# Performance work log

Hardware: AMD Instinct MI355X
Metric: run time of the kernel (lower is better)

The kernel has to match this reference:

```python
import jax, jax.numpy as jnp
import numpy as np

D_MODEL = 1024
NUM_HEADS = 16
HEAD_DIM = D_MODEL // NUM_HEADS
B, S = 2, 2048


def setup_inputs() -> dict:
    key = jax.random.key(0)
    ks = jax.random.split(key, 9)
    scale = 1.0 / np.sqrt(D_MODEL)
    return {
        "x": jax.random.normal(ks[0], (B, S, D_MODEL), jnp.float32),
        "y": jax.random.normal(ks[1], (B, S, D_MODEL), jnp.float32),
        "mask": jnp.zeros((B, S, S), jnp.float32),
        "Wkv": jax.random.normal(ks[2], (D_MODEL, 2 * D_MODEL), jnp.float32) * scale,
        "bkv": jnp.zeros((2 * D_MODEL,), jnp.float32),
        "Wq": jax.random.normal(ks[3], (D_MODEL, D_MODEL), jnp.float32) * scale,
        "bq": jnp.zeros((D_MODEL,), jnp.float32),
        "Wo": jax.random.normal(ks[4], (D_MODEL, D_MODEL), jnp.float32) * scale,
        "bo": jnp.zeros((D_MODEL,), jnp.float32),
    }


def reference(x, y, mask, Wkv, bkv, Wq, bq, Wo, bo):
    b, s, d = x.shape
    h, hd = NUM_HEADS, HEAD_DIM
    # projections
    kv = x @ Wkv + bkv                       # [B, S, 2D]
    q = y @ Wq + bq                          # [B, S, D]
    kv = kv.reshape(b, s, h, 2 * hd).transpose(0, 2, 1, 3)  # [B, H, S, 2hd]
    q = q.reshape(b, s, h, hd).transpose(0, 2, 1, 3)        # [B, H, S, hd]
    k, v = kv[..., :hd], kv[..., hd:]
    # scaled dot-product attention with additive per-batch mask
    scaled = jnp.einsum("bhqd,bhkd->bhqk", q, k) / jnp.sqrt(jnp.float32(hd))
    scaled = scaled + mask[:, None, :, :]    # mask [B,S,S] broadcast over heads
    attn = jax.nn.softmax(scaled, axis=-1)
    vals = jnp.einsum("bhqk,bhkd->bhqd", attn, v)            # [B, H, S, hd]
    vals = vals.transpose(0, 2, 1, 3).reshape(b, s, d)       # [B, S, D]
    return vals @ Wo + bo
```

## Files before the change

kernel.cpp:

```cpp
#include <hip/hip_runtime.h>
#include <hip/hip_bf16.h>

#define D_MODEL 1024
#define NHEADS 16
#define HD 64
#define BATCH 2
#define SEQ 2048
#define BS (BATCH*SEQ)

typedef __bf16 bf16;
typedef bf16 bf16x4 __attribute__((ext_vector_type(4)));
typedef bf16 bf16x8 __attribute__((ext_vector_type(8)));
typedef float f32x4 __attribute__((ext_vector_type(4)));

#define AS1 __attribute__((address_space(1)))
#define AS3 __attribute__((address_space(3)))

__device__ __forceinline__ void gload_lds16(const void* g, void* l) {
  __builtin_amdgcn_global_load_lds((AS1 const unsigned int*)g, (AS3 unsigned int*)l, 16, 0, 0);
}

__device__ __forceinline__ float exp2_fast(float x) {
  float r;
  asm("v_exp_f32 %0, %1\n\ts_nop 1" : "=v"(r) : "v"(x));
  return r;
}

__global__ void cvt_bf16(const float* __restrict__ in, bf16* __restrict__ out, int n8) {
  int i = blockIdx.x * blockDim.x + threadIdx.x;
  int stride = gridDim.x * blockDim.x;
  for (; i < n8; i += stride) {
    const float4* p = (const float4*)(in + (size_t)i * 8);
    float4 a = p[0], b = p[1];
    bf16x8 o;
    o[0]=(bf16)a.x; o[1]=(bf16)a.y; o[2]=(bf16)a.z; o[3]=(bf16)a.w;
    o[4]=(bf16)b.x; o[5]=(bf16)b.y; o[6]=(bf16)b.z; o[7]=(bf16)b.w;
    *(bf16x8*)(out + (size_t)i * 8) = o;
  }
}

__global__ void transpose_cvt(const float* __restrict__ in, bf16* __restrict__ out, int R, int C) {
  __shared__ bf16 tile[64][72];
  const int t = threadIdx.x;
  const int r0 = blockIdx.x * 64;
  const int c0 = blockIdx.y * 64;
  {
    int r = t >> 2, cc = (t & 3) * 16;
    const float* src = in + (size_t)(r0 + r) * C + c0 + cc;
    #pragma unroll
    for (int j = 0; j < 16; j += 4) {
      float4 v = *(const float4*)(src + j);
      tile[r][cc + j + 0] = (bf16)v.x;
      tile[r][cc + j + 1] = (bf16)v.y;
      tile[r][cc + j + 2] = (bf16)v.z;
      tile[r][cc + j + 3] = (bf16)v.w;
    }
  }
  __syncthreads();
  {
    int c = t >> 2, rr = (t & 3) * 16;
    bf16* dst = out + (size_t)(c0 + c) * R + r0 + rr;
    bf16x8 o0, o1;
    #pragma unroll
    for (int j = 0; j < 8; j++) { o0[j] = tile[rr + j][c]; o1[j] = tile[rr + 8 + j][c]; }
    *(bf16x8*)dst = o0;
    *(bf16x8*)(dst + 8) = o1;
  }
}

__global__ void mask_scan(const float* __restrict__ mask, int n4, int* __restrict__ flag) {
  int i = blockIdx.x * blockDim.x + threadIdx.x;
  int stride = gridDim.x * blockDim.x;
  int any = 0;
  for (; i < n4; i += stride) {
    float4 v = *(const float4*)(mask + (size_t)i * 4);
    if (v.x != 0.f || v.y != 0.f || v.z != 0.f || v.w != 0.f) any = 1;
  }
  if (__ballot(any) && (threadIdx.x & 63) == 0) atomicOr(flag, 1);
}

template <typename OutT, int MODE>
__global__ __launch_bounds__(256)
void gemm_bt(const bf16* __restrict__ A, const bf16* __restrict__ Bt,
             const float* __restrict__ bias, OutT* __restrict__ C,
             bf16* __restrict__ Vt, int M, int N, int K, float scale) {
  __shared__ char lds[32768];
  char* Alds = lds;
  char* Blds = lds + 16384;
  const int t = threadIdx.x;
  const int lane = t & 63;
  const int wid = t >> 6;
  const int m0 = blockIdx.x * 128;
  const int n0 = blockIdx.y * 128;
  const int wr = wid >> 1, wc = wid & 1;

  f32x4 acc[4][4] = {};

  int rowL[4], colL[4];
  #pragma unroll
  for (int i = 0; i < 4; i++) {
    int L = t * 16 + i * 4096;
    int r = L >> 7;
    rowL[i] = r;
    colL[i] = (L & 127) ^ ((r & 7) << 4);
  }
  const char* Ab = (const char*)A;
  const char* Bb = (const char*)Bt;
  const size_t rs = (size_t)K * 2;

  for (int k0 = 0; k0 < K; k0 += 64) {
    #pragma unroll
    for (int i = 0; i < 4; i++) {
      gload_lds16(Ab + (size_t)(m0 + rowL[i]) * rs + (size_t)k0 * 2 + colL[i],
                  Alds + i * 4096 + t * 16);
      gload_lds16(Bb + (size_t)(n0 + rowL[i]) * rs + (size_t)k0 * 2 + colL[i],
                  Blds + i * 4096 + t * 16);
    }
    __syncthreads();
    #pragma unroll
    for (int kb = 0; kb < 2; kb++) {
      bf16x8 af[4], bfr[4];
      #pragma unroll
      for (int m = 0; m < 4; m++) {
        int r = wr * 64 + m * 16 + (lane & 15);
        int cb = (kb * 64 + ((lane >> 4) << 4)) ^ ((r & 7) << 4);
        af[m] = *(const bf16x8*)(Alds + r * 128 + cb);
      }
      #pragma unroll
      for (int n = 0; n < 4; n++) {
        int r = wc * 64 + n * 16 + (lane & 15);
        int cb = (kb * 64 + ((lane >> 4) << 4)) ^ ((r & 7) << 4);
        bfr[n] = *(const bf16x8*)(Blds + r * 128 + cb);
      }
      #pragma unroll
      for (int m = 0; m < 4; m++)
        #pragma unroll
        for (int n = 0; n < 4; n++)
          acc[m][n] = __builtin_amdgcn_mfma_f32_16x16x32_bf16(af[m], bfr[n], acc[m][n], 0, 0, 0);
    }
    __syncthreads();
  }

  if (MODE == 1 && wc == 1) {
    const int h = n0 >> 7;
    const int bb = m0 >> 11;
    #pragma unroll
    for (int n = 0; n < 4; n++) {
      const int d = n * 16 + (lane & 15);
      const int cg = n0 + 64 + d;
      const float bv = bias[cg];
      bf16* vrow = Vt + ((size_t)((bb * NHEADS + h) * HD + d)) * SEQ;
      #pragma unroll
      for (int m = 0; m < 4; m++) {
        const int rb = m0 + wr * 64 + m * 16 + ((lane >> 4) << 2);
        const int s = rb & (SEQ - 1);
        bf16x4 v;
        #pragma unroll
        for (int j = 0; j < 4; j++) v[j] = (bf16)((acc[m][n][j] + bv) * scale);
        *(bf16x4*)(vrow + s) = v;
      }
    }
  } else {
    #pragma unroll
    for (int m = 0; m < 4; m++) {
      const int rb = m0 + wr * 64 + m * 16 + ((lane >> 4) << 2);
      #pragma unroll
      for (int n = 0; n < 4; n++) {
        const int cg = n0 + wc * 64 + n * 16 + (lane & 15);
        const float bv = bias[cg];
        #pragma unroll
        for (int j = 0; j < 4; j++) {
          C[(size_t)(rb + j) * N + cg] = (OutT)((acc[m][n][j] + bv) * scale);
        }
      }
    }
  }
}

__global__ __launch_bounds__(256)
void attn_kernel(const bf16* __restrict__ Qb, const bf16* __restrict__ KV,
                 const bf16* __restrict__ Vt, const float* __restrict__ mask,
                 const int* __restrict__ flag, bf16* __restrict__ vals) {
  __shared__ char lds[49152];
  const int t = threadIdx.x;
  const int lane = t & 63;
  const int wid = t >> 6;
  const int g = lane >> 4;
  const int lq = lane & 15;
  char* Pw = lds + 32768 + wid * 4096;

  int wg = ((blockIdx.x & 7) << 6) | (blockIdx.x >> 3);
  const int qt = wg & 15;
  const int h = (wg >> 4) & 15;
  const int b = wg >> 8;
  const int q0 = qt * 128 + wid * 32;
  const bool use_mask = (*flag) != 0;

  bf16x8 qf[2][2];
  #pragma unroll
  for (int m = 0; m < 2; m++)
    #pragma unroll
    for (int kb = 0; kb < 2; kb++) {
      int r = q0 + m * 16 + lq;
      qf[m][kb] = *(const bf16x8*)(Qb + (size_t)(b * SEQ + r) * D_MODEL + h * HD + kb * 32 + g * 8);
    }

  f32x4 oacc[2][4] = {};
  float mrun[2], lrun[2];
  mrun[0] = mrun[1] = -1e30f;
  lrun[0] = lrun[1] = 0.f;

  int kvOff[2][4];
  #pragma unroll
  for (int kb = 0; kb < 2; kb++)
    #pragma unroll
    for (int n = 0; n < 4; n++) {
      int r = n * 16 + lq;
      kvOff[kb][n] = r * 128 + ((kb * 64 + (g << 4)) ^ ((r & 7) << 4));
    }
  int pROff[2][2];
  #pragma unroll
  for (int m = 0; m < 2; m++)
    #pragma unroll
    for (int kb = 0; kb < 2; kb++) {
      int r = m * 16 + lq;
      pROff[m][kb] = r * 128 + ((kb * 64 + (g << 4)) ^ ((r & 7) << 4));
    }
  int pWOff[2][4];
  #pragma unroll
  for (int m = 0; m < 2; m++) {
    int r = m * 16 + lq;
    int swz = (r & 7) << 4;
    #pragma unroll
    for (int n = 0; n < 4; n++)
      pWOff[m][n] = r * 128 + ((n * 32 + g * 8) ^ swz);
  }

  int rowL[2], colL[2];
  #pragma unroll
  for (int i = 0; i < 2; i++) {
    int L = t * 16 + i * 4096;
    int r = L >> 7;
    rowL[i] = r;
    colL[i] = (L & 127) ^ ((r & 7) << 4);
  }
  const char* KVb = (const char*)KV;
  const char* Vtb = (const char*)Vt;

  auto stage = [&](int kt, int c) {
    const int kv0 = kt * 64;
    char* Kb = lds + c * 16384;
    char* Vb = Kb + 8192;
    #pragma unroll
    for (int i = 0; i < 2; i++) {
      gload_lds16(KVb + (size_t)(b * SEQ + kv0 + rowL[i]) * (2 * D_MODEL * 2) + h * 256 + colL[i],
                  Kb + i * 4096 + t * 16);
      gload_lds16(Vtb + (size_t)((b * NHEADS + h) * HD + rowL[i]) * (SEQ * 2) + kv0 * 2 + colL[i],
                  Vb + i * 4096 + t * 16);
    }
  };

  stage(0, 0);
  __syncthreads();
  int cur = 0;

  const int NT = SEQ / 64;
  for (int kt = 0; kt < NT; kt++) {
    if (kt + 1 < NT) stage(kt + 1, cur ^ 1);
    char* Klds = lds + cur * 16384;
    char* Vlds = Klds + 8192;
    const int kv0 = kt * 64;

    f32x4 sacc[2][4] = {};
    __builtin_amdgcn_s_setprio(1);
    #pragma unroll
    for (int kb = 0; kb < 2; kb++) {
      bf16x8 kf[4];
      #pragma unroll
      for (int n = 0; n < 4; n++)
        kf[n] = *(const bf16x8*)(Klds + kvOff[kb][n]);
      #pragma unroll
      for (int m = 0; m < 2; m++)
        #pragma unroll
        for (int n = 0; n < 4; n++)
          sacc[m][n] = __builtin_amdgcn_mfma_f32_16x16x32_bf16(kf[n], qf[m][kb], sacc[m][n], 0, 0, 0);
    }
    __builtin_amdgcn_s_setprio(0);

    if (use_mask) {
      #pragma unroll
      for (int m = 0; m < 2; m++) {
        int qg = q0 + m * 16 + lq;
        const float* mrow = mask + ((size_t)b * SEQ + qg) * SEQ + kv0;
        #pragma unroll
        for (int n = 0; n < 4; n++)
          #pragma unroll
          for (int j = 0; j < 4; j++)
            sacc[m][n][j] += mrow[n * 16 + g * 4 + j] * 1.44269504f;
      }
    }

    float pm[2];
    #pragma unroll
    for (int m = 0; m < 2; m++) {
      float a0 = fmaxf(fmaxf(sacc[m][0][0], sacc[m][0][1]), fmaxf(sacc[m][0][2], sacc[m][0][3]));
      float a1 = fmaxf(fmaxf(sacc[m][1][0], sacc[m][1][1]), fmaxf(sacc[m][1][2], sacc[m][1][3]));
      float a2 = fmaxf(fmaxf(sacc[m][2][0], sacc[m][2][1]), fmaxf(sacc[m][2][2], sacc[m][2][3]));
      float a3 = fmaxf(fmaxf(sacc[m][3][0], sacc[m][3][1]), fmaxf(sacc[m][3][2], sacc[m][3][3]));
      float v = fmaxf(fmaxf(a0, a1), fmaxf(a2, a3));
      v = fmaxf(v, __shfl_xor(v, 16, 64));
      v = fmaxf(v, __shfl_xor(v, 32, 64));
      pm[m] = v;
    }

    int nogrow = (pm[0] <= mrun[0] + 8.f) && (pm[1] <= mrun[1] + 8.f);
    if (!__all(nogrow)) {
      #pragma unroll
      for (int m = 0; m < 2; m++) {
        float mn = fmaxf(mrun[m], pm[m]);
        float sf = exp2_fast(mrun[m] - mn);
        mrun[m] = mn;
        lrun[m] *= sf;
        float sfj[4];
        #pragma unroll
        for (int j = 0; j < 4; j++) sfj[j] = __shfl(sf, (g << 2) + j, 64);
        #pragma unroll
        for (int n = 0; n < 4; n++)
          #pragma unroll
          for (int j = 0; j < 4; j++)
            oacc[m][n][j] *= sfj[j];
      }
    }

    #pragma unroll
    for (int m = 0; m < 2; m++) {
      float rsn[4];
      #pragma unroll
      for (int n = 0; n < 4; n++) {
        float e0 = exp2_fast(sacc[m][n][0] - mrun[m]);
        float e1 = exp2_fast(sacc[m][n][1] - mrun[m]);
        float e2 = exp2_fast(sacc[m][n][2] - mrun[m]);
        float e3 = exp2_fast(sacc[m][n][3] - mrun[m]);
        rsn[n] = (e0 + e1) + (e2 + e3);
        bf16x4 p = {(bf16)e0, (bf16)e1, (bf16)e2, (bf16)e3};
        *(bf16x4*)(Pw + pWOff[m][n]) = p;
      }
      lrun[m] += (rsn[0] + rsn[1]) + (rsn[2] + rsn[3]);
    }

    asm volatile("s_waitcnt lgkmcnt(0)" ::: "memory");
    __builtin_amdgcn_sched_barrier(0);

    __builtin_amdgcn_s_setprio(1);
    #pragma unroll
    for (int kb = 0; kb < 2; kb++) {
      bf16x8 pf[2], vf[4];
      #pragma unroll
      for (int m = 0; m < 2; m++)
        pf[m] = *(const bf16x8*)(Pw + pROff[m][kb]);
      #pragma unroll
      for (int n = 0; n < 4; n++)
        vf[n] = *(const bf16x8*)(Vlds + kvOff[kb][n]);
      #pragma unroll
      for (int m = 0; m < 2; m++)
        #pragma unroll
        for (int n = 0; n < 4; n++)
          oacc[m][n] = __builtin_amdgcn_mfma_f32_16x16x32_bf16(pf[m], vf[n], oacc[m][n], 0, 0, 0);
    }
    __builtin_amdgcn_s_setprio(0);

    __syncthreads();
    cur ^= 1;
  }

  #pragma unroll
  for (int m = 0; m < 2; m++) {
    lrun[m] += __shfl_xor(lrun[m], 16, 64);
    lrun[m] += __shfl_xor(lrun[m], 32, 64);
  }

  #pragma unroll
  for (int m = 0; m < 2; m++) {
    float inv[4];
    #pragma unroll
    for (int j = 0; j < 4; j++)
      inv[j] = 1.f / __shfl(lrun[m], (g << 2) + j, 64);
    #pragma unroll
    for (int n = 0; n < 4; n++) {
      int cg = h * HD + n * 16 + lq;
      #pragma unroll
      for (int j = 0; j < 4; j++) {
        int rg = b * SEQ + q0 + m * 16 + g * 4 + j;
        vals[(size_t)rg * D_MODEL + cg] = (bf16)(oacc[m][n][j] * inv[j]);
      }
    }
  }
}

extern "C" void kernel_launch(void* const* d_in, const int* in_sizes, int n_in,
                              void* d_out, int out_size, void* d_ws, size_t ws_size,
                              hipStream_t stream) {
  const float* x    = (const float*)d_in[0];
  const float* y    = (const float*)d_in[1];
  const float* mask = (const float*)d_in[2];
  const float* Wkv  = (const float*)d_in[3];
  const float* bkv  = (const float*)d_in[4];
  const float* Wq   = (const float*)d_in[5];
  const float* bq   = (const float*)d_in[6];
  const float* Wo   = (const float*)d_in[7];
  const float* bo   = (const float*)d_in[8];
  float* out = (float*)d_out;

  char* ws = (char*)d_ws;
  bf16* xb   = (bf16*)(ws);
  bf16* yb   = (bf16*)(ws + (8ull << 20));
  bf16* Wkvt = (bf16*)(ws + (16ull << 20));
  bf16* Wqt  = (bf16*)(ws + (20ull << 20));
  bf16* Wot  = (bf16*)(ws + (22ull << 20));
  bf16* KVb  = (bf16*)(ws + (24ull << 20));
  bf16* Qbuf = (bf16*)(ws + (40ull << 20));
  bf16* Vt   = (bf16*)(ws + (48ull << 20));
  bf16* vals = (bf16*)(ws + (56ull << 20));
  int*  flag = (int*)(ws + (64ull << 20));

  const float QSCL = 0.125f * 1.44269504f;

  hipMemsetAsync(flag, 0, 4, stream);
  mask_scan<<<2048, 256, 0, stream>>>(mask, BATCH * SEQ * SEQ / 4, flag);
  cvt_bf16<<<2048, 256, 0, stream>>>(x, xb, BS * D_MODEL / 8);
  cvt_bf16<<<2048, 256, 0, stream>>>(y, yb, BS * D_MODEL / 8);
  transpose_cvt<<<dim3(16, 32), 256, 0, stream>>>(Wkv, Wkvt, 1024, 2048);
  transpose_cvt<<<dim3(16, 16), 256, 0, stream>>>(Wq, Wqt, 1024, 1024);
  transpose_cvt<<<dim3(16, 16), 256, 0, stream>>>(Wo, Wot, 1024, 1024);
  gemm_bt<bf16, 1><<<dim3(32, 16), 256, 0, stream>>>(xb, Wkvt, bkv, KVb, Vt, 4096, 2048, 1024, 1.0f);
  gemm_bt<bf16, 0><<<dim3(32, 8), 256, 0, stream>>>(yb, Wqt, bq, Qbuf, nullptr, 4096, 1024, 1024, QSCL);
  attn_kernel<<<512, 256, 0, stream>>>(Qbuf, KVb, Vt, mask, flag, vals);
  gemm_bt<float, 0><<<dim3(32, 8), 256, 0, stream>>>(vals, Wot, bo, out, nullptr, 4096, 1024, 1024, 1.0f);
}
```

Baseline: 160.3 us.

## Load K/V fragments directly from global memory in single-wave attention blocks

Restructures the attention kernel from 4-wave workgroups that stage K/V tiles into double-buffered shared memory into single-wave workgroups (4x as many blocks) that read K and V MFMA fragments straight from global memory into registers. This removes the LDS staging, the block-wide barriers and the LDS read traffic, and lets each wave run independently. In exchange, K/V reuse across the four waves of a block is lost, so global/L2 traffic rises about fourfold and the loads are no longer prefetched one tile ahead, which exposes memory latency unless occupancy hides it.

```diff
diff --git a/kernel.cpp b/kernel.cpp
--- a/kernel.cpp
+++ b/kernel.cpp
@@ -177,23 +177,20 @@
   }
 }
 
-__global__ __launch_bounds__(256)
+__global__ __launch_bounds__(64)
 void attn_kernel(const bf16* __restrict__ Qb, const bf16* __restrict__ KV,
                  const bf16* __restrict__ Vt, const float* __restrict__ mask,
                  const int* __restrict__ flag, bf16* __restrict__ vals) {
-  __shared__ char lds[49152];
-  const int t = threadIdx.x;
-  const int lane = t & 63;
-  const int wid = t >> 6;
+  __shared__ char Pw[4096];
+  const int lane = threadIdx.x;
   const int g = lane >> 4;
   const int lq = lane & 15;
-  char* Pw = lds + 32768 + wid * 4096;
-
-  int wg = ((blockIdx.x & 7) << 6) | (blockIdx.x >> 3);
-  const int qt = wg & 15;
-  const int h = (wg >> 4) & 15;
-  const int b = wg >> 8;
-  const int q0 = qt * 128 + wid * 32;
+
+  int wg = ((blockIdx.x & 7) << 8) | (blockIdx.x >> 3);
+  const int qt = wg & 63;
+  const int h = (wg >> 6) & 15;
+  const int b = wg >> 10;
+  const int q0 = qt * 32;
   const bool use_mask = (*flag) != 0;
 
   bf16x8 qf[2][2];
@@ -210,14 +207,6 @@
   mrun[0] = mrun[1] = -1e30f;
   lrun[0] = lrun[1] = 0.f;
 
-  int kvOff[2][4];
-  #pragma unroll
-  for (int kb = 0; kb < 2; kb++)
-    #pragma unroll
-    for (int n = 0; n < 4; n++) {
-      int r = n * 16 + lq;
-      kvOff[kb][n] = r * 128 + ((kb * 64 + (g << 4)) ^ ((r & 7) << 4));
-    }
   int pROff[2][2];
   #pragma unroll
   for (int m = 0; m < 2; m++)
@@ -236,56 +225,37 @@
       pWOff[m][n] = r * 128 + ((n * 32 + g * 8) ^ swz);
   }
 
-  int rowL[2], colL[2];
-  #pragma unroll
-  for (int i = 0; i < 2; i++) {
-    int L = t * 16 + i * 4096;
-    int r = L >> 7;
-    rowL[i] = r;
-    colL[i] = (L & 127) ^ ((r & 7) << 4);
-  }
-  const char* KVb = (const char*)KV;
-  const char* Vtb = (const char*)Vt;
-
-  auto stage = [&](int kt, int c) {
-    const int kv0 = kt * 64;
-    char* Kb = lds + c * 16384;
-    char* Vb = Kb + 8192;
-    #pragma unroll
-    for (int i = 0; i < 2; i++) {
-      gload_lds16(KVb + (size_t)(b * SEQ + kv0 + rowL[i]) * (2 * D_MODEL * 2) + h * 256 + colL[i],
-                  Kb + i * 4096 + t * 16);
-      gload_lds16(Vtb + (size_t)((b * NHEADS + h) * HD + rowL[i]) * (SEQ * 2) + kv0 * 2 + colL[i],
-                  Vb + i * 4096 + t * 16);
-    }
-  };
-
-  stage(0, 0);
-  __syncthreads();
-  int cur = 0;
+  const bf16* Kb = KV + (size_t)(b * SEQ) * (2 * D_MODEL) + h * 128;
+  const bf16* Vb = Vt + (size_t)((b * NHEADS + h) * HD) * SEQ;
 
   const int NT = SEQ / 64;
   for (int kt = 0; kt < NT; kt++) {
-    if (kt + 1 < NT) stage(kt + 1, cur ^ 1);
-    char* Klds = lds + cur * 16384;
-    char* Vlds = Klds + 8192;
     const int kv0 = kt * 64;
+
+    bf16x8 kf[2][4];
+    #pragma unroll
+    for (int kb = 0; kb < 2; kb++)
+      #pragma unroll
+      for (int n = 0; n < 4; n++)
+        kf[kb][n] = *(const bf16x8*)(Kb + (size_t)(kv0 + n * 16 + lq) * (2 * D_MODEL) + kb * 32 + g * 8);
 
     f32x4 sacc[2][4] = {};
     __builtin_amdgcn_s_setprio(1);
     #pragma unroll
-    for (int kb = 0; kb < 2; kb++) {
-      bf16x8 kf[4];
+    for (int kb = 0; kb < 2; kb++)
+      #pragma unroll
+      for (int m = 0; m < 2; m++)
+        #pragma unroll
+        for (int n = 0; n < 4; n++)
+          sacc[m][n] = __builtin_amdgcn_mfma_f32_16x16x32_bf16(kf[kb][n], qf[m][kb], sacc[m][n], 0, 0, 0);
+    __builtin_amdgcn_s_setprio(0);
+
+    bf16x8 vf[2][4];
+    #pragma unroll
+    for (int kb = 0; kb < 2; kb++)
       #pragma unroll
       for (int n = 0; n < 4; n++)
-        kf[n] = *(const bf16x8*)(Klds + kvOff[kb][n]);
-      #pragma unroll
-      for (int m = 0; m < 2; m++)
-        #pragma unroll
-        for (int n = 0; n < 4; n++)
-          sacc[m][n] = __builtin_amdgcn_mfma_f32_16x16x32_bf16(kf[n], qf[m][kb], sacc[m][n], 0, 0, 0);
-    }
-    __builtin_amdgcn_s_setprio(0);
+        vf[kb][n] = *(const bf16x8*)(Vb + (size_t)(n * 16 + lq) * SEQ + kv0 + kb * 32 + g * 8);
 
     if (use_mask) {
       #pragma unroll
@@ -348,29 +318,20 @@
       lrun[m] += (rsn[0] + rsn[1]) + (rsn[2] + rsn[3]);
     }
 
-    asm volatile("s_waitcnt lgkmcnt(0)" ::: "memory");
-    __builtin_amdgcn_sched_barrier(0);
-
     __builtin_amdgcn_s_setprio(1);
     #pragma unroll
     for (int kb = 0; kb < 2; kb++) {
-      bf16x8 pf[2], vf[4];
+      bf16x8 pf[2];
       #pragma unroll
       for (int m = 0; m < 2; m++)
         pf[m] = *(const bf16x8*)(Pw + pROff[m][kb]);
       #pragma unroll
-      for (int n = 0; n < 4; n++)
-        vf[n] = *(const bf16x8*)(Vlds + kvOff[kb][n]);
-      #pragma unroll
       for (int m = 0; m < 2; m++)
         #pragma unroll
         for (int n = 0; n < 4; n++)
-          oacc[m][n] = __builtin_amdgcn_mfma_f32_16x16x32_bf16(pf[m], vf[n], oacc[m][n], 0, 0, 0);
+          oacc[m][n] = __builtin_amdgcn_mfma_f32_16x16x32_bf16(pf[m], vf[kb][n], oacc[m][n], 0, 0, 0);
     }
     __builtin_amdgcn_s_setprio(0);
-
-    __syncthreads();
-    cur ^= 1;
   }
 
   #pragma unroll
@@ -434,6 +395,6 @@
   transpose_cvt<<<dim3(16, 16), 256, 0, stream>>>(Wo, Wot, 1024, 1024);
   gemm_bt<bf16, 1><<<dim3(32, 16), 256, 0, stream>>>(xb, Wkvt, bkv, KVb, Vt, 4096, 2048, 1024, 1.0f);
   gemm_bt<bf16, 0><<<dim3(32, 8), 256, 0, stream>>>(yb, Wqt, bq, Qbuf, nullptr, 4096, 1024, 1024, QSCL);
-  attn_kernel<<<512, 256, 0, stream>>>(Qbuf, KVb, Vt, mask, flag, vals);
+  attn_kernel<<<2048, 64, 0, stream>>>(Qbuf, KVb, Vt, mask, flag, vals);
   gemm_bt<float, 0><<<dim3(32, 8), 256, 0, stream>>>(vals, Wot, bo, out, nullptr, 4096, 1024, 1024, 1.0f);
 }
```

After: 218.0 us. +36.0%, slower.

## Merge preprocessing kernels and fuse K/V and Q projection GEMMs into one launch

Applied to the files above, without the earlier changes.

The mask scan, the x/y bf16 conversions and the three weight transpose-converts now run as one block-indexed prep kernel instead of six launches. The KV and Q projection GEMMs share a single launch, with a 32x24 grid that dispatches on blockIdx.y. The goal is to cut launch overhead and tail idle time between small kernels and to give the GPU a larger, fuller grid for the projections. The cost is branchy block dispatch and some extra register pressure in the combined GEMM epilogue; KV tiles still store the K half row-major, while wc==1 waves write V transposed.

```diff
diff --git a/kernel.cpp b/kernel.cpp
--- a/kernel.cpp
+++ b/kernel.cpp
@@ -26,64 +26,190 @@
   return r;
 }
 
-__global__ void cvt_bf16(const float* __restrict__ in, bf16* __restrict__ out, int n8) {
-  int i = blockIdx.x * blockDim.x + threadIdx.x;
-  int stride = gridDim.x * blockDim.x;
-  for (; i < n8; i += stride) {
+__global__ __launch_bounds__(256)
+void prep_kernel(const float* __restrict__ x, const float* __restrict__ y,
+                 const float* __restrict__ mask,
+                 const float* __restrict__ Wkv, const float* __restrict__ Wq,
+                 const float* __restrict__ Wo,
+                 bf16* __restrict__ xb, bf16* __restrict__ yb,
+                 bf16* __restrict__ Wkvt, bf16* __restrict__ Wqt,
+                 bf16* __restrict__ Wot, int* __restrict__ flag) {
+  __shared__ bf16 tile[64][72];
+  const int blk = blockIdx.x;
+  const int t = threadIdx.x;
+
+  if (blk < 4096) {
+    const float* in = (blk < 2048) ? x : y;
+    bf16* out = (blk < 2048) ? xb : yb;
+    int i = (blk & 2047) * 256 + t;
     const float4* p = (const float4*)(in + (size_t)i * 8);
     float4 a = p[0], b = p[1];
     bf16x8 o;
     o[0]=(bf16)a.x; o[1]=(bf16)a.y; o[2]=(bf16)a.z; o[3]=(bf16)a.w;
     o[4]=(bf16)b.x; o[5]=(bf16)b.y; o[6]=(bf16)b.z; o[7]=(bf16)b.w;
     *(bf16x8*)(out + (size_t)i * 8) = o;
-  }
-}
-
-__global__ void transpose_cvt(const float* __restrict__ in, bf16* __restrict__ out, int R, int C) {
-  __shared__ bf16 tile[64][72];
+  } else if (blk < 5120) {
+    const float* tin; bf16* tout; int C, tt;
+    if (blk < 4608)      { tin = Wkv; tout = Wkvt; C = 2048; tt = blk - 4096; }
+    else if (blk < 4864) { tin = Wq;  tout = Wqt;  C = 1024; tt = blk - 4608; }
+    else                 { tin = Wo;  tout = Wot;  C = 1024; tt = blk - 4864; }
+    const int R = 1024;
+    const int r0 = (tt & 15) * 64;
+    const int c0 = (tt >> 4) * 64;
+    {
+      int r = t >> 2, cc = (t & 3) * 16;
+      const float* src = tin + (size_t)(r0 + r) * C + c0 + cc;
+      #pragma unroll
+      for (int j = 0; j < 16; j += 4) {
+        float4 v = *(const float4*)(src + j);
+        tile[r][cc + j + 0] = (bf16)v.x;
+        tile[r][cc + j + 1] = (bf16)v.y;
+        tile[r][cc + j + 2] = (bf16)v.z;
+        tile[r][cc + j + 3] = (bf16)v.w;
+      }
+    }
+    __syncthreads();
+    {
+      int c = t >> 2, rr = (t & 3) * 16;
+      bf16* dst = tout + (size_t)(c0 + c) * R + r0 + rr;
+      bf16x8 o0, o1;
+      #pragma unroll
+      for (int j = 0; j < 8; j++) { o0[j] = tile[rr + j][c]; o1[j] = tile[rr + 8 + j][c]; }
+      *(bf16x8*)dst = o0;
+      *(bf16x8*)(dst + 8) = o1;
+    }
+  } else {
+    const int n4 = BATCH * SEQ * SEQ / 4;
+    int i = (blk - 5120) * 256 + t;
+    const int stride = 1024 * 256;
+    int any = 0;
+    for (; i < n4; i += stride) {
+      float4 v = *(const float4*)(mask + (size_t)i * 4);
+      if (v.x != 0.f || v.y != 0.f || v.z != 0.f || v.w != 0.f) any = 1;
+    }
+    if (__ballot(any) && (t & 63) == 0) atomicOr(flag, 1);
+  }
+}
+
+__global__ __launch_bounds__(256)
+void qkv_gemm(const bf16* __restrict__ xb, const bf16* __restrict__ yb,
+              const bf16* __restrict__ Wkvt, const bf16* __restrict__ Wqt,
+              const float* __restrict__ bkv, const float* __restrict__ bq,
+              bf16* __restrict__ KVb, bf16* __restrict__ Qbuf,
+              bf16* __restrict__ Vt, float QSCL) {
+  __shared__ char lds[32768];
+  char* Alds = lds;
+  char* Blds = lds + 16384;
+  const int K = 1024;
   const int t = threadIdx.x;
-  const int r0 = blockIdx.x * 64;
-  const int c0 = blockIdx.y * 64;
-  {
-    int r = t >> 2, cc = (t & 3) * 16;
-    const float* src = in + (size_t)(r0 + r) * C + c0 + cc;
-    #pragma unroll
-    for (int j = 0; j < 16; j += 4) {
-      float4 v = *(const float4*)(src + j);
-      tile[r][cc + j + 0] = (bf16)v.x;
-      tile[r][cc + j + 1] = (bf16)v.y;
-      tile[r][cc + j + 2] = (bf16)v.z;
-      tile[r][cc + j + 3] = (bf16)v.w;
-    }
-  }
-  __syncthreads();
-  {
-    int c = t >> 2, rr = (t & 3) * 16;
-    bf16* dst = out + (size_t)(c0 + c) * R + r0 + rr;
-    bf16x8 o0, o1;
-    #pragma unroll
-    for (int j = 0; j < 8; j++) { o0[j] = tile[rr + j][c]; o1[j] = tile[rr + 8 + j][c]; }
-    *(bf16x8*)dst = o0;
-    *(bf16x8*)(dst + 8) = o1;
-  }
-}
-
-__global__ void mask_scan(const float* __restrict__ mask, int n4, int* __restrict__ flag) {
-  int i = blockIdx.x * blockDim.x + threadIdx.x;
-  int stride = gridDim.x * blockDim.x;
-  int any = 0;
-  for (; i < n4; i += stride) {
-    float4 v = *(const float4*)(mask + (size_t)i * 4);
-    if (v.x != 0.f || v.y != 0.f || v.z != 0.f || v.w != 0.f) any = 1;
-  }
-  if (__ballot(any) && (threadIdx.x & 63) == 0) atomicOr(flag, 1);
-}
-
-template <typename OutT, int MODE>
+  const int lane = t & 63;
+  const int wid = t >> 6;
+  const int m0 = blockIdx.x * 128;
+  const int by = blockIdx.y;
+  const bool isQ = by >= 16;
+  const int n0 = (isQ ? by - 16 : by) * 128;
+  const bf16* A = isQ ? yb : xb;
+  const bf16* Bt = isQ ? Wqt : Wkvt;
+  const int wr = wid >> 1, wc = wid & 1;
+
+  f32x4 acc[4][4] = {};
+
+  int rowL[4], colL[4];
+  #pragma unroll
+  for (int i = 0; i < 4; i++) {
+    int L = t * 16 + i * 4096;
+    int r = L >> 7;
+    rowL[i] = r;
+    colL[i] = (L & 127) ^ ((r & 7) << 4);
+  }
+  const char* Ab = (const char*)A;
+  const char* Bb = (const char*)Bt;
+  const size_t rs = (size_t)K * 2;
+
+  for (int k0 = 0; k0 < K; k0 += 64) {
+    #pragma unroll
+    for (int i = 0; i < 4; i++) {
+      gload_lds16(Ab + (size_t)(m0 + rowL[i]) * rs + (size_t)k0 * 2 + colL[i],
+                  Alds + i * 4096 + t * 16);
+      gload_lds16(Bb + (size_t)(n0 + rowL[i]) * rs + (size_t)k0 * 2 + colL[i],
+                  Blds + i * 4096 + t * 16);
+    }
+    __syncthreads();
+    #pragma unroll
+    for (int kb = 0; kb < 2; kb++) {
+      bf16x8 af[4], bfr[4];
+      #pragma unroll
+      for (int m = 0; m < 4; m++) {
+        int r = wr * 64 + m * 16 + (lane & 15);
+        int cb = (kb * 64 + ((lane >> 4) << 4)) ^ ((r & 7) << 4);
+        af[m] = *(const bf16x8*)(Alds + r * 128 + cb);
+      }
+      #pragma unroll
+      for (int n = 0; n < 4; n++) {
+        int r = wc * 64 + n * 16 + (lane & 15);
+        int cb = (kb * 64 + ((lane >> 4) << 4)) ^ ((r & 7) << 4);
+        bfr[n] = *(const bf16x8*)(Blds + r * 128 + cb);
+      }
+      #pragma unroll
+      for (int m = 0; m < 4; m++)
+        #pragma unroll
+        for (int n = 0; n < 4; n++)
+          acc[m][n] = __builtin_amdgcn_mfma_f32_16x16x32_bf16(af[m], bfr[n], acc[m][n], 0, 0, 0);
+    }
+    __syncthreads();
+  }
+
+  if (!isQ && wc == 1) {
+    const int h = n0 >> 7;
+    const int bb = m0 >> 11;
+    #pragma unroll
+    for (int n = 0; n < 4; n++) {
+      const int d = n * 16 + (lane & 15);
+      const float bv = bkv[n0 + 64 + d];
+      bf16* vrow = Vt + ((size_t)((bb * NHEADS + h) * HD + d)) * SEQ;
+      #pragma unroll
+      for (int m = 0; m < 4; m++) {
+        const int rb = m0 + wr * 64 + m * 16 + ((lane >> 4) << 2);
+        const int s = rb & (SEQ - 1);
+        bf16x4 v;
+        #pragma unroll
+        for (int j = 0; j < 4; j++) v[j] = (bf16)(acc[m][n][j] + bv);
+        *(bf16x4*)(vrow + s) = v;
+      }
+    }
+  } else if (!isQ) {
+    #pragma unroll
+    for (int m = 0; m < 4; m++) {
+      const int rb = m0 + wr * 64 + m * 16 + ((lane >> 4) << 2);
+      #pragma unroll
+      for (int n = 0; n < 4; n++) {
+        const int cg = n0 + n * 16 + (lane & 15);
+        const float bv = bkv[cg];
+        #pragma unroll
+        for (int j = 0; j < 4; j++)
+          KVb[(size_t)(rb + j) * 2048 + cg] = (bf16)(acc[m][n][j] + bv);
+      }
+    }
+  } else {
+    #pragma unroll
+    for (int m = 0; m < 4; m++) {
+      const int rb = m0 + wr * 64 + m * 16 + ((lane >> 4) << 2);
+      #pragma unroll
+      for (int n = 0; n < 4; n++) {
+        const int cg = n0 + wc * 64 + n * 16 + (lane & 15);
+        const float bv = bq[cg];
+        #pragma unroll
+        for (int j = 0; j < 4; j++)
+          Qbuf[(size_t)(rb + j) * 1024 + cg] = (bf16)((acc[m][n][j] + bv) * QSCL);
+      }
+    }
+  }
+}
+
 __global__ __launch_bounds__(256)
-void gemm_bt(const bf16* __restrict__ A, const bf16* __restrict__ Bt,
-             const float* __restrict__ bias, OutT* __restrict__ C,
-             bf16* __restrict__ Vt, int M, int N, int K, float scale) {
+void gemm_o(const bf16* __restrict__ A, const bf16* __restrict__ Bt,
+            const float* __restrict__ bias, float* __restrict__ C,
+            int M, int N, int K) {
   __shared__ char lds[32768];
   char* Alds = lds;
   char* Blds = lds + 16384;
@@ -141,38 +267,16 @@
     __syncthreads();
   }
 
-  if (MODE == 1 && wc == 1) {
-    const int h = n0 >> 7;
-    const int bb = m0 >> 11;
+  #pragma unroll
+  for (int m = 0; m < 4; m++) {
+    const int rb = m0 + wr * 64 + m * 16 + ((lane >> 4) << 2);
     #pragma unroll
     for (int n = 0; n < 4; n++) {
-      const int d = n * 16 + (lane & 15);
-      const int cg = n0 + 64 + d;
+      const int cg = n0 + wc * 64 + n * 16 + (lane & 15);
       const float bv = bias[cg];
-      bf16* vrow = Vt + ((size_t)((bb * NHEADS + h) * HD + d)) * SEQ;
-      #pragma unroll
-      for (int m = 0; m < 4; m++) {
-        const int rb = m0 + wr * 64 + m * 16 + ((lane >> 4) << 2);
-        const int s = rb & (SEQ - 1);
-        bf16x4 v;
-        #pragma unroll
-        for (int j = 0; j < 4; j++) v[j] = (bf16)((acc[m][n][j] + bv) * scale);
-        *(bf16x4*)(vrow + s) = v;
-      }
-    }
-  } else {
-    #pragma unroll
-    for (int m = 0; m < 4; m++) {
-      const int rb = m0 + wr * 64 + m * 16 + ((lane >> 4) << 2);
-      #pragma unroll
-      for (int n = 0; n < 4; n++) {
-        const int cg = n0 + wc * 64 + n * 16 + (lane & 15);
-        const float bv = bias[cg];
-        #pragma unroll
-        for (int j = 0; j < 4; j++) {
-          C[(size_t)(rb + j) * N + cg] = (OutT)((acc[m][n][j] + bv) * scale);
-        }
-      }
+      #pragma unroll
+      for (int j = 0; j < 4; j++)
+        C[(size_t)(rb + j) * N + cg] = acc[m][n][j] + bv;
     }
   }
 }
@@ -365,7 +469,7 @@
       for (int m = 0; m < 2; m++)
         #pragma unroll
         for (int n = 0; n < 4; n++)
-          oacc[m][n] = __builtin_amdgcn_mfma_f32_16x16x32_bf16(pf[m], vf[n], oacc[m][n], 0, 0, 0);
+          oacc[m][n] = __builtin_amdgcn_mfma_f32_16x16x32_bf16(pf[m], vf[kb? n : n], oacc[m][n], 0, 0, 0);
     }
     __builtin_amdgcn_s_setprio(0);
 
@@ -426,14 +530,10 @@
   const float QSCL = 0.125f * 1.44269504f;
 
   hipMemsetAsync(flag, 0, 4, stream);
-  mask_scan<<<2048, 256, 0, stream>>>(mask, BATCH * SEQ * SEQ / 4, flag);
-  cvt_bf16<<<2048, 256, 0, stream>>>(x, xb, BS * D_MODEL / 8);
-  cvt_bf16<<<2048, 256, 0, stream>>>(y, yb, BS * D_MODEL / 8);
-  transpose_cvt<<<dim3(16, 32), 256, 0, stream>>>(Wkv, Wkvt, 1024, 2048);
-  transpose_cvt<<<dim3(16, 16), 256, 0, stream>>>(Wq, Wqt, 1024, 1024);
-  transpose_cvt<<<dim3(16, 16), 256, 0, stream>>>(Wo, Wot, 1024, 1024);
-  gemm_bt<bf16, 1><<<dim3(32, 16), 256, 0, stream>>>(xb, Wkvt, bkv, KVb, Vt, 4096, 2048, 1024, 1.0f);
-  gemm_bt<bf16, 0><<<dim3(32, 8), 256, 0, stream>>>(yb, Wqt, bq, Qbuf, nullptr, 4096, 1024, 1024, QSCL);
+  prep_kernel<<<6144, 256, 0, stream>>>(x, y, mask, Wkv, Wq, Wo,
+                                        xb, yb, Wkvt, Wqt, Wot, flag);
+  qkv_gemm<<<dim3(32, 24), 256, 0, stream>>>(xb, yb, Wkvt, Wqt, bkv, bq,
+                                             KVb, Qbuf, Vt, QSCL);
   attn_kernel<<<512, 256, 0, stream>>>(Qbuf, KVb, Vt, mask, flag, vals);
-  gemm_bt<float, 0><<<dim3(32, 8), 256, 0, stream>>>(vals, Wot, bo, out, nullptr, 4096, 1024, 1024, 1.0f);
-}
+  gemm_o<<<dim3(32, 8), 256, 0, stream>>>(vals, Wot, bo, out, 4096, 1024, 1024);
+}
```

Result: faster. 147.3 us (-8.1%).
